# Kernel optimization log

Measured on AMD Instinct MI355X. Metric: run time of the kernel, lower is better.

Reference implementation:

```python
import jax, jax.numpy as jnp
import numpy as np

B, C, H, W = 32, 512, 64, 64
K = 32  # num_codes


def setup_inputs() -> dict:
    key = jax.random.key(0)
    k1, k2, k3 = jax.random.split(key, 3)
    x = jax.random.normal(k1, (B, C, H, W), dtype=jnp.float32)
    std = 1.0 / (K * C) ** 0.5
    codewords = jax.random.uniform(k2, (K, C), dtype=jnp.float32, minval=-std, maxval=std)
    scale = jax.random.uniform(k3, (K,), dtype=jnp.float32, minval=-1.0, maxval=0.0)
    return {"x": x, "codewords": codewords, "scale": scale}


def reference(x, codewords, scale):
    # x: [B, C, H, W] -> [B, N, C] with N = H*W
    b, c = x.shape[0], x.shape[1]
    xf = x.reshape(b, c, -1).transpose(0, 2, 1)  # [B, N, C]
    # scaled L2: scale_k * ||x_n - c_k||^2, expanded algebraically to avoid [B,N,K,C]
    x2 = jnp.sum(xf * xf, axis=-1)                      # [B, N]
    c2 = jnp.sum(codewords * codewords, axis=-1)        # [K]
    xc = jnp.einsum('bnc,kc->bnk', xf, codewords)       # [B, N, K]
    dist = scale[None, None, :] * (x2[:, :, None] - 2.0 * xc + c2[None, None, :])
    w = jax.nn.softmax(dist, axis=2)                    # [B, N, K]
    # aggregate: sum_n w_{nk} * (x_n - c_k) = (w^T x) - (sum_n w_{nk}) * c_k
    wx = jnp.einsum('bnk,bnc->bkc', w, xf)              # [B, K, C]
    wsum = jnp.sum(w, axis=1)                           # [B, K]
    encoded_feat = wx - wsum[:, :, None] * codewords[None, :, :]  # [B, K, C]
    return encoded_feat
```

## Files before the change

kernel.cpp:

```cpp
#include <hip/hip_runtime.h>
#include <stdint.h>

#define Bdim 32
#define Cdim 512
#define Ndim 4096
#define Kdim 32
#define NPX 32
#define NCH 16
#define PWIN 8

static constexpr size_t WS_WSUM_OFF = (size_t)256 * Kdim * Cdim * 4;
static constexpr size_t WS_C2_OFF   = WS_WSUM_OFF + (size_t)256 * Kdim * 4;

using bf16x8 = __attribute__((ext_vector_type(8))) short;
using f32x4  = __attribute__((ext_vector_type(4))) float;

static __device__ __forceinline__ unsigned short f2bf(float f) {
    unsigned int u = __float_as_uint(f);
    u += 0x7fffu + ((u >> 16) & 1u);
    return (unsigned short)(u >> 16);
}

__global__ __launch_bounds__(256) void k0_c2(const float* __restrict__ cw,
                                             float* __restrict__ c2) {
    __shared__ float partl[8][32];
    int t = threadIdx.x;
    int k = t & 31, g = t >> 5;
    float s = 0.f;
    int c0 = g * 64;
    for (int c = c0; c < c0 + 64; ++c) {
        float v = cw[k * Cdim + c];
        s += v * v;
    }
    partl[g][k] = s;
    __syncthreads();
    if (t < 32) {
        float tot = 0.f;
        #pragma unroll
        for (int gg = 0; gg < 8; ++gg) tot += partl[gg][t];
        c2[t] = tot;
    }
}

__global__ __launch_bounds__(512, 2) void k1_fused(const float* __restrict__ x,
                                                   const float* __restrict__ cw,
                                                   const float* __restrict__ scale,
                                                   const float* __restrict__ c2g,
                                                   float* __restrict__ part,
                                                   float* __restrict__ wsum_part) {
    __shared__ unsigned short cw_s[Kdim][520];
    __shared__ unsigned short x_n[NPX][520];
    __shared__ unsigned short x_t[Cdim][40];
    __shared__ float          S_s[2][NPX][36];
    __shared__ unsigned short w_t[Kdim][40];
    __shared__ float          x2_w[8][NPX];
    __shared__ float          wsum_w[4][Kdim];

    const int t    = threadIdx.x;
    const int blk  = blockIdx.x;
    const int b    = blk >> 3;
    const int pw   = blk & 7;
    const int lane = t & 63;
    const int lr   = lane & 15;
    const int lq   = lane >> 4;
    const int wv   = t >> 6;
    const int pp   = t & 15;
    const int crg  = t >> 4;
    const int q    = t & 7;
    const int px   = t >> 3;
    const int pt   = wv & 1;
    const int kt2  = (wv >> 1) & 1;
    const int ch   = wv >> 2;

    #pragma unroll
    for (int i = 0; i < 8; ++i) {
        int f4 = t + 512 * i;
        int k  = f4 >> 7;
        int c4 = (f4 & 127) * 4;
        float4 v = *(const float4*)(cw + (size_t)k * Cdim + c4);
        ushort4 u;
        u.x = f2bf(v.x); u.y = f2bf(v.y); u.z = f2bf(v.z); u.w = f2bf(v.w);
        *(ushort4*)&cw_s[k][c4] = u;
    }

    float4 sc4, c24;
    if (t < 256) {
        sc4 = *(const float4*)(scale + 4 * q);
        c24 = *(const float4*)(c2g + 4 * q);
    }

    const float* xb = x + (size_t)b * Cdim * Ndim;

    float2 pa[8], pb[8];
    {
        int n0 = pw * 512;
        #pragma unroll
        for (int i = 0; i < 8; ++i) {
            int c = 2 * crg + 64 * i;
            pa[i] = *(const float2*)(xb + (size_t)c * Ndim + n0 + 2 * pp);
            pb[i] = *(const float2*)(xb + (size_t)(c + 1) * Ndim + n0 + 2 * pp);
        }
    }

    f32x4 acc[2][4];
    #pragma unroll
    for (int kt = 0; kt < 2; ++kt)
        #pragma unroll
        for (int ct = 0; ct < 4; ++ct) acc[kt][ct] = (f32x4){0.f, 0.f, 0.f, 0.f};
    float wsum_r[4] = {0.f, 0.f, 0.f, 0.f};

    __syncthreads();

    for (int ci = 0; ci < NCH; ++ci) {
        float x2p0 = 0.f, x2p1 = 0.f;
        #pragma unroll
        for (int i = 0; i < 8; ++i) {
            int c = 2 * crg + 64 * i;
            float2 a = pa[i], bb = pb[i];
            unsigned short ax = f2bf(a.x), ay = f2bf(a.y);
            unsigned short bx = f2bf(bb.x), by = f2bf(bb.y);
            ushort2 u;
            u.x = ax; u.y = ay; *(ushort2*)&x_t[c][2 * pp] = u;
            u.x = bx; u.y = by; *(ushort2*)&x_t[c + 1][2 * pp] = u;
            u.x = ax; u.y = bx; *(ushort2*)&x_n[2 * pp][c] = u;
            u.x = ay; u.y = by; *(ushort2*)&x_n[2 * pp + 1][c] = u;
            x2p0 += a.x * a.x + bb.x * bb.x;
            x2p1 += a.y * a.y + bb.y * bb.y;
        }
        x2p0 += __shfl_xor(x2p0, 16); x2p1 += __shfl_xor(x2p1, 16);
        x2p0 += __shfl_xor(x2p0, 32); x2p1 += __shfl_xor(x2p1, 32);
        if (lane < 16) {
            float2 v; v.x = x2p0; v.y = x2p1;
            *(float2*)&x2_w[wv][2 * pp] = v;
        }
        if (ci + 1 < NCH) {
            int nn = pw * 512 + (ci + 1) * 32;
            #pragma unroll
            for (int i = 0; i < 8; ++i) {
                int c = 2 * crg + 64 * i;
                pa[i] = *(const float2*)(xb + (size_t)c * Ndim + nn + 2 * pp);
                pb[i] = *(const float2*)(xb + (size_t)(c + 1) * Ndim + nn + 2 * pp);
            }
        }
        __syncthreads();

        {
            f32x4 d = (f32x4){0.f, 0.f, 0.f, 0.f};
            #pragma unroll
            for (int s = 0; s < 8; ++s) {
                int col = 256 * ch + 32 * s + 8 * lq;
                bf16x8 av = *(const bf16x8*)&x_n[16 * pt + lr][col];
                bf16x8 bv = *(const bf16x8*)&cw_s[16 * kt2 + lr][col];
                d = __builtin_amdgcn_mfma_f32_16x16x32_bf16(av, bv, d, 0, 0, 0);
            }
            #pragma unroll
            for (int r = 0; r < 4; ++r)
                S_s[ch][16 * pt + 4 * lq + r][16 * kt2 + lr] = d[r];
        }
        __syncthreads();

        if (t < 256) {
            float4 dv0 = *(const float4*)&S_s[0][px][4 * q];
            float4 dv1 = *(const float4*)&S_s[1][px][4 * q];
            float xx = 0.f;
            #pragma unroll
            for (int w = 0; w < 8; ++w) xx += x2_w[w][px];
            float d0 = sc4.x * (xx - 2.f * (dv0.x + dv1.x) + c24.x);
            float d1 = sc4.y * (xx - 2.f * (dv0.y + dv1.y) + c24.y);
            float d2 = sc4.z * (xx - 2.f * (dv0.z + dv1.z) + c24.z);
            float d3 = sc4.w * (xx - 2.f * (dv0.w + dv1.w) + c24.w);
            float m = fmaxf(fmaxf(d0, d1), fmaxf(d2, d3));
            m = fmaxf(m, __shfl_xor(m, 1));
            m = fmaxf(m, __shfl_xor(m, 2));
            m = fmaxf(m, __shfl_xor(m, 4));
            float e0 = __expf(d0 - m), e1 = __expf(d1 - m);
            float e2 = __expf(d2 - m), e3 = __expf(d3 - m);
            float ss = e0 + e1 + e2 + e3;
            ss += __shfl_xor(ss, 1);
            ss += __shfl_xor(ss, 2);
            ss += __shfl_xor(ss, 4);
            float inv = 1.f / ss;
            float w0 = e0 * inv, w1 = e1 * inv, w2 = e2 * inv, w3 = e3 * inv;
            wsum_r[0] += w0; wsum_r[1] += w1; wsum_r[2] += w2; wsum_r[3] += w3;
            w_t[4 * q + 0][px] = f2bf(w0);
            w_t[4 * q + 1][px] = f2bf(w1);
            w_t[4 * q + 2][px] = f2bf(w2);
            w_t[4 * q + 3][px] = f2bf(w3);
        }
        __syncthreads();

        {
            bf16x8 a0 = *(const bf16x8*)&w_t[lr][8 * lq];
            bf16x8 a1 = *(const bf16x8*)&w_t[16 + lr][8 * lq];
            #pragma unroll
            for (int ct = 0; ct < 4; ++ct) {
                bf16x8 bv = *(const bf16x8*)&x_t[64 * wv + 16 * ct + lr][8 * lq];
                acc[0][ct] = __builtin_amdgcn_mfma_f32_16x16x32_bf16(a0, bv, acc[0][ct], 0, 0, 0);
                acc[1][ct] = __builtin_amdgcn_mfma_f32_16x16x32_bf16(a1, bv, acc[1][ct], 0, 0, 0);
            }
        }
        __syncthreads();
    }

    if (t < 256) {
        #pragma unroll
        for (int j = 0; j < 4; ++j) {
            float v = wsum_r[j];
            v += __shfl_xor(v, 8);
            v += __shfl_xor(v, 16);
            v += __shfl_xor(v, 32);
            if (lane < 8) wsum_w[wv][4 * lane + j] = v;
        }
    }
    {
        float* pbuf = part + (size_t)blk * (Kdim * Cdim);
        #pragma unroll
        for (int kt = 0; kt < 2; ++kt)
            #pragma unroll
            for (int ct = 0; ct < 4; ++ct)
                #pragma unroll
                for (int r = 0; r < 4; ++r)
                    pbuf[(size_t)(16 * kt + 4 * lq + r) * Cdim + 64 * wv + 16 * ct + lr] =
                        acc[kt][ct][r];
    }
    __syncthreads();
    if (t < 32) {
        float s = wsum_w[0][t] + wsum_w[1][t] + wsum_w[2][t] + wsum_w[3][t];
        wsum_part[blk * Kdim + t] = s;
    }
}

__global__ __launch_bounds__(256) void k2_reduce(const float* __restrict__ part,
                                                 const float* __restrict__ wsum_part,
                                                 const float* __restrict__ cw,
                                                 float* __restrict__ out) {
    int blk = blockIdx.x;
    int b = blk >> 5, k = blk & 31;
    int t = threadIdx.x;
    float ws = 0.f;
    #pragma unroll
    for (int p = 0; p < PWIN; ++p) ws += wsum_part[(b * PWIN + p) * Kdim + k];
    int c = 2 * t;
    float sx = 0.f, sy = 0.f;
    #pragma unroll
    for (int p = 0; p < PWIN; ++p) {
        const float2 v = *(const float2*)(part + ((size_t)(b * PWIN + p) * Kdim + k) * Cdim + c);
        sx += v.x;
        sy += v.y;
    }
    float2 cv = *(const float2*)(cw + (size_t)k * Cdim + c);
    float2 o;
    o.x = sx - ws * cv.x;
    o.y = sy - ws * cv.y;
    *(float2*)(out + ((size_t)b * Kdim + k) * Cdim + c) = o;
}

extern "C" void kernel_launch(void* const* d_in, const int* in_sizes, int n_in,
                              void* d_out, int out_size, void* d_ws, size_t ws_size,
                              hipStream_t stream) {
    const float* x     = (const float*)d_in[0];
    const float* cw    = (const float*)d_in[1];
    const float* scale = (const float*)d_in[2];
    float* out = (float*)d_out;

    char* wsb = (char*)d_ws;
    float* part      = (float*)wsb;
    float* wsum_part = (float*)(wsb + WS_WSUM_OFF);
    float* c2        = (float*)(wsb + WS_C2_OFF);

    k0_c2<<<1, 256, 0, stream>>>(cw, c2);
    k1_fused<<<Bdim * PWIN, 512, 0, stream>>>(x, cw, scale, c2, part, wsum_part);
    k2_reduce<<<Bdim * Kdim, 256, 0, stream>>>(part, wsum_part, cw, out);
}
```

Baseline: 381.6 us.

## Halve pixel tile, hold codewords in registers, batch aggregation GEMM over two chunks

The fused kernel now uses 256-thread blocks that each process 16 pixels per chunk, and the grid doubles to 16 pixel windows per batch. Each wave keeps its codeword fragments in registers instead of a shared-memory copy. The x_t and w_t tiles are double-buffered by chunk parity, so the weighted-sum MFMA runs once per two chunks with a full 32-wide K dimension, which removes one barrier per chunk. The trade-off is twice as many partial results for the reduce kernel to write and read, plus higher register pressure from the larger accumulator array.

Measured after the change: 392.6 us. 1.03x slower.

```diff
diff --git a/kernel.cpp b/kernel.cpp
--- a/kernel.cpp
+++ b/kernel.cpp
@@ -5,12 +5,12 @@
 #define Cdim 512
 #define Ndim 4096
 #define Kdim 32
-#define NPX 32
+#define NPX 16
 #define NCH 16
-#define PWIN 8
-
-static constexpr size_t WS_WSUM_OFF = (size_t)256 * Kdim * Cdim * 4;
-static constexpr size_t WS_C2_OFF   = WS_WSUM_OFF + (size_t)256 * Kdim * 4;
+#define PWIN 16
+
+static constexpr size_t WS_WSUM_OFF = (size_t)512 * Kdim * Cdim * 4;
+static constexpr size_t WS_C2_OFF   = WS_WSUM_OFF + (size_t)512 * Kdim * 4;
 
 using bf16x8 = __attribute__((ext_vector_type(8))) short;
 using f32x4  = __attribute__((ext_vector_type(4))) float;
@@ -42,76 +42,76 @@
     }
 }
 
-__global__ __launch_bounds__(512, 2) void k1_fused(const float* __restrict__ x,
+__global__ __launch_bounds__(256, 2) void k1_fused(const float* __restrict__ x,
                                                    const float* __restrict__ cw,
                                                    const float* __restrict__ scale,
                                                    const float* __restrict__ c2g,
                                                    float* __restrict__ part,
                                                    float* __restrict__ wsum_part) {
-    __shared__ unsigned short cw_s[Kdim][520];
     __shared__ unsigned short x_n[NPX][520];
     __shared__ unsigned short x_t[Cdim][40];
     __shared__ float          S_s[2][NPX][36];
     __shared__ unsigned short w_t[Kdim][40];
-    __shared__ float          x2_w[8][NPX];
-    __shared__ float          wsum_w[4][Kdim];
+    __shared__ float          x2_w[4][NPX];
+    __shared__ float          wsum_w[2][Kdim];
 
     const int t    = threadIdx.x;
     const int blk  = blockIdx.x;
-    const int b    = blk >> 3;
-    const int pw   = blk & 7;
+    const int b    = blk >> 4;
+    const int pw   = blk & 15;
     const int lane = t & 63;
     const int lr   = lane & 15;
     const int lq   = lane >> 4;
     const int wv   = t >> 6;
-    const int pp   = t & 15;
-    const int crg  = t >> 4;
+    const int pp   = t & 7;
+    const int crg  = t >> 3;
     const int q    = t & 7;
     const int px   = t >> 3;
-    const int pt   = wv & 1;
-    const int kt2  = (wv >> 1) & 1;
-    const int ch   = wv >> 2;
-
-    #pragma unroll
-    for (int i = 0; i < 8; ++i) {
-        int f4 = t + 512 * i;
-        int k  = f4 >> 7;
-        int c4 = (f4 & 127) * 4;
-        float4 v = *(const float4*)(cw + (size_t)k * Cdim + c4);
-        ushort4 u;
-        u.x = f2bf(v.x); u.y = f2bf(v.y); u.z = f2bf(v.z); u.w = f2bf(v.w);
-        *(ushort4*)&cw_s[k][c4] = u;
+    const int kt2  = wv & 1;
+    const int ch   = wv >> 1;
+
+    bf16x8 cwf[8];
+    {
+        const float* cr = cw + (size_t)(16 * kt2 + lr) * Cdim + 256 * ch + 8 * lq;
+        #pragma unroll
+        for (int s = 0; s < 8; ++s) {
+            float4 v0 = *(const float4*)(cr + 32 * s);
+            float4 v1 = *(const float4*)(cr + 32 * s + 4);
+            bf16x8 f;
+            f[0] = (short)f2bf(v0.x); f[1] = (short)f2bf(v0.y);
+            f[2] = (short)f2bf(v0.z); f[3] = (short)f2bf(v0.w);
+            f[4] = (short)f2bf(v1.x); f[5] = (short)f2bf(v1.y);
+            f[6] = (short)f2bf(v1.z); f[7] = (short)f2bf(v1.w);
+            cwf[s] = f;
+        }
     }
 
     float4 sc4, c24;
-    if (t < 256) {
+    if (t < 128) {
         sc4 = *(const float4*)(scale + 4 * q);
         c24 = *(const float4*)(c2g + 4 * q);
     }
 
-    const float* xb = x + (size_t)b * Cdim * Ndim;
+    const float* xb = x + (size_t)b * Cdim * Ndim + pw * (NPX * NCH);
 
     float2 pa[8], pb[8];
-    {
-        int n0 = pw * 512;
-        #pragma unroll
-        for (int i = 0; i < 8; ++i) {
-            int c = 2 * crg + 64 * i;
-            pa[i] = *(const float2*)(xb + (size_t)c * Ndim + n0 + 2 * pp);
-            pb[i] = *(const float2*)(xb + (size_t)(c + 1) * Ndim + n0 + 2 * pp);
-        }
-    }
-
-    f32x4 acc[2][4];
+    #pragma unroll
+    for (int i = 0; i < 8; ++i) {
+        int c = 2 * crg + 64 * i;
+        pa[i] = *(const float2*)(xb + (size_t)c * Ndim + 2 * pp);
+        pb[i] = *(const float2*)(xb + (size_t)(c + 1) * Ndim + 2 * pp);
+    }
+
+    f32x4 acc[2][8];
     #pragma unroll
     for (int kt = 0; kt < 2; ++kt)
         #pragma unroll
-        for (int ct = 0; ct < 4; ++ct) acc[kt][ct] = (f32x4){0.f, 0.f, 0.f, 0.f};
+        for (int ct = 0; ct < 8; ++ct) acc[kt][ct] = (f32x4){0.f, 0.f, 0.f, 0.f};
     float wsum_r[4] = {0.f, 0.f, 0.f, 0.f};
 
-    __syncthreads();
-
     for (int ci = 0; ci < NCH; ++ci) {
+        const int par = (ci & 1) * NPX;
+
         float x2p0 = 0.f, x2p1 = 0.f;
         #pragma unroll
         for (int i = 0; i < 8; ++i) {
@@ -120,51 +120,49 @@
             unsigned short ax = f2bf(a.x), ay = f2bf(a.y);
             unsigned short bx = f2bf(bb.x), by = f2bf(bb.y);
             ushort2 u;
-            u.x = ax; u.y = ay; *(ushort2*)&x_t[c][2 * pp] = u;
-            u.x = bx; u.y = by; *(ushort2*)&x_t[c + 1][2 * pp] = u;
+            u.x = ax; u.y = ay; *(ushort2*)&x_t[c][par + 2 * pp] = u;
+            u.x = bx; u.y = by; *(ushort2*)&x_t[c + 1][par + 2 * pp] = u;
             u.x = ax; u.y = bx; *(ushort2*)&x_n[2 * pp][c] = u;
             u.x = ay; u.y = by; *(ushort2*)&x_n[2 * pp + 1][c] = u;
             x2p0 += a.x * a.x + bb.x * bb.x;
             x2p1 += a.y * a.y + bb.y * bb.y;
         }
+        x2p0 += __shfl_xor(x2p0, 8);  x2p1 += __shfl_xor(x2p1, 8);
         x2p0 += __shfl_xor(x2p0, 16); x2p1 += __shfl_xor(x2p1, 16);
         x2p0 += __shfl_xor(x2p0, 32); x2p1 += __shfl_xor(x2p1, 32);
-        if (lane < 16) {
+        if (lane < 8) {
             float2 v; v.x = x2p0; v.y = x2p1;
             *(float2*)&x2_w[wv][2 * pp] = v;
         }
+        __syncthreads();
+
         if (ci + 1 < NCH) {
-            int nn = pw * 512 + (ci + 1) * 32;
+            const float* xn2 = xb + (ci + 1) * NPX;
             #pragma unroll
             for (int i = 0; i < 8; ++i) {
                 int c = 2 * crg + 64 * i;
-                pa[i] = *(const float2*)(xb + (size_t)c * Ndim + nn + 2 * pp);
-                pb[i] = *(const float2*)(xb + (size_t)(c + 1) * Ndim + nn + 2 * pp);
+                pa[i] = *(const float2*)(xn2 + (size_t)c * Ndim + 2 * pp);
+                pb[i] = *(const float2*)(xn2 + (size_t)(c + 1) * Ndim + 2 * pp);
             }
         }
-        __syncthreads();
 
         {
             f32x4 d = (f32x4){0.f, 0.f, 0.f, 0.f};
             #pragma unroll
             for (int s = 0; s < 8; ++s) {
-                int col = 256 * ch + 32 * s + 8 * lq;
-                bf16x8 av = *(const bf16x8*)&x_n[16 * pt + lr][col];
-                bf16x8 bv = *(const bf16x8*)&cw_s[16 * kt2 + lr][col];
-                d = __builtin_amdgcn_mfma_f32_16x16x32_bf16(av, bv, d, 0, 0, 0);
+                bf16x8 av = *(const bf16x8*)&x_n[lr][256 * ch + 32 * s + 8 * lq];
+                d = __builtin_amdgcn_mfma_f32_16x16x32_bf16(av, cwf[s], d, 0, 0, 0);
             }
             #pragma unroll
             for (int r = 0; r < 4; ++r)
-                S_s[ch][16 * pt + 4 * lq + r][16 * kt2 + lr] = d[r];
+                S_s[ch][4 * lq + r][16 * kt2 + lr] = d[r];
         }
         __syncthreads();
 
-        if (t < 256) {
+        if (t < 128) {
             float4 dv0 = *(const float4*)&S_s[0][px][4 * q];
             float4 dv1 = *(const float4*)&S_s[1][px][4 * q];
-            float xx = 0.f;
-            #pragma unroll
-            for (int w = 0; w < 8; ++w) xx += x2_w[w][px];
+            float xx = x2_w[0][px] + x2_w[1][px] + x2_w[2][px] + x2_w[3][px];
             float d0 = sc4.x * (xx - 2.f * (dv0.x + dv1.x) + c24.x);
             float d1 = sc4.y * (xx - 2.f * (dv0.y + dv1.y) + c24.y);
             float d2 = sc4.z * (xx - 2.f * (dv0.z + dv1.z) + c24.z);
@@ -182,27 +180,27 @@
             float inv = 1.f / ss;
             float w0 = e0 * inv, w1 = e1 * inv, w2 = e2 * inv, w3 = e3 * inv;
             wsum_r[0] += w0; wsum_r[1] += w1; wsum_r[2] += w2; wsum_r[3] += w3;
-            w_t[4 * q + 0][px] = f2bf(w0);
-            w_t[4 * q + 1][px] = f2bf(w1);
-            w_t[4 * q + 2][px] = f2bf(w2);
-            w_t[4 * q + 3][px] = f2bf(w3);
+            w_t[4 * q + 0][par + px] = f2bf(w0);
+            w_t[4 * q + 1][par + px] = f2bf(w1);
+            w_t[4 * q + 2][par + px] = f2bf(w2);
+            w_t[4 * q + 3][par + px] = f2bf(w3);
         }
         __syncthreads();
 
-        {
+        if (ci & 1) {
             bf16x8 a0 = *(const bf16x8*)&w_t[lr][8 * lq];
             bf16x8 a1 = *(const bf16x8*)&w_t[16 + lr][8 * lq];
             #pragma unroll
-            for (int ct = 0; ct < 4; ++ct) {
-                bf16x8 bv = *(const bf16x8*)&x_t[64 * wv + 16 * ct + lr][8 * lq];
+            for (int ct = 0; ct < 8; ++ct) {
+                bf16x8 bv = *(const bf16x8*)&x_t[128 * wv + 16 * ct + lr][8 * lq];
                 acc[0][ct] = __builtin_amdgcn_mfma_f32_16x16x32_bf16(a0, bv, acc[0][ct], 0, 0, 0);
                 acc[1][ct] = __builtin_amdgcn_mfma_f32_16x16x32_bf16(a1, bv, acc[1][ct], 0, 0, 0);
             }
-        }
-        __syncthreads();
-    }
-
-    if (t < 256) {
+            __syncthreads();
+        }
+    }
+
+    if (t < 128) {
         #pragma unroll
         for (int j = 0; j < 4; ++j) {
             float v = wsum_r[j];
@@ -217,17 +215,14 @@
         #pragma unroll
         for (int kt = 0; kt < 2; ++kt)
             #pragma unroll
-            for (int ct = 0; ct < 4; ++ct)
+            for (int ct = 0; ct < 8; ++ct)
                 #pragma unroll
                 for (int r = 0; r < 4; ++r)
-                    pbuf[(size_t)(16 * kt + 4 * lq + r) * Cdim + 64 * wv + 16 * ct + lr] =
+                    pbuf[(size_t)(16 * kt + 4 * lq + r) * Cdim + 128 * wv + 16 * ct + lr] =
                         acc[kt][ct][r];
     }
     __syncthreads();
-    if (t < 32) {
-        float s = wsum_w[0][t] + wsum_w[1][t] + wsum_w[2][t] + wsum_w[3][t];
-        wsum_part[blk * Kdim + t] = s;
-    }
+    if (t < 32) wsum_part[blk * Kdim + t] = wsum_w[0][t] + wsum_w[1][t];
 }
 
 __global__ __launch_bounds__(256) void k2_reduce(const float* __restrict__ part,
@@ -269,6 +264,6 @@
     float* c2        = (float*)(wsb + WS_C2_OFF);
 
     k0_c2<<<1, 256, 0, stream>>>(cw, c2);
-    k1_fused<<<Bdim * PWIN, 512, 0, stream>>>(x, cw, scale, c2, part, wsum_part);
+    k1_fused<<<Bdim * PWIN, 256, 0, stream>>>(x, cw, scale, c2, part, wsum_part);
     k2_reduce<<<Bdim * Kdim, 256, 0, stream>>>(part, wsum_part, cw, out);
 }
```
